# Optimization experiments

Measured on AMD Instinct MI355X. Metric: run time of the kernel, lower is better.

Reference implementation:

```python
import jax, jax.numpy as jnp
import numpy as np

H = 2048
D = 128            # align_dim
TEMP_TAU = 1.0
BIAS_MAX = 0.5
LN_EPS = 1e-5


def _ln(x, g, b):
    m = jnp.mean(x, axis=-1, keepdims=True)
    v = jnp.mean((x - m) ** 2, axis=-1, keepdims=True)
    return (x - m) / jnp.sqrt(v + LN_EPS) * g + b


def _mlp(x, g, b, W1, b1, W2, b2):
    # LayerNorm -> Linear -> GELU(exact) -> Linear
    h = jax.nn.gelu(_ln(x, g, b) @ W1.T + b1, approximate=False)
    return h @ W2.T + b2


def _l2n(x):
    n = jnp.linalg.norm(x, axis=-1, keepdims=True)
    return x / jnp.maximum(n, 1e-12)


def setup_inputs() -> dict:
    key = jax.random.key(0)
    ks = jax.random.split(key, 20)
    B, L = 4096, 4096
    d2 = 2 * D
    s_h = 1.0 / np.sqrt(H)
    s_d2 = 1.0 / np.sqrt(d2)
    inp = {
        "q": jax.random.normal(ks[0], (B, H), jnp.float32),
        "R_non": jax.random.normal(ks[1], (L, H), jnp.float32),
        # mlp_q
        "ln_q_g": jnp.ones((H,), jnp.float32),
        "ln_q_b": jnp.zeros((H,), jnp.float32),
        "W1q": jax.random.uniform(ks[2], (d2, H), jnp.float32, -s_h, s_h),
        "b1q": jnp.zeros((d2,), jnp.float32),
        "W2q": jax.random.uniform(ks[3], (D, d2), jnp.float32, -s_d2, s_d2),
        "b2q": jnp.zeros((D,), jnp.float32),
        # mlp_r
        "ln_r_g": jnp.ones((H,), jnp.float32),
        "ln_r_b": jnp.zeros((H,), jnp.float32),
        "W1r": jax.random.uniform(ks[4], (d2, H), jnp.float32, -s_h, s_h),
        "b1r": jnp.zeros((d2,), jnp.float32),
        "W2r": jax.random.uniform(ks[5], (D, d2), jnp.float32, -s_d2, s_d2),
        "b2r": jnp.zeros((D,), jnp.float32),
        # mlp_dec (input 2D=256 -> 128 -> 1)
        "ln_d_g": jnp.ones((d2,), jnp.float32),
        "ln_d_b": jnp.zeros((d2,), jnp.float32),
        "W1d": jax.random.uniform(ks[6], (128, d2), jnp.float32, -s_d2, s_d2),
        "b1d": jnp.zeros((128,), jnp.float32),
        "W2d": jax.random.uniform(ks[7], (1, 128), jnp.float32, -1 / np.sqrt(128), 1 / np.sqrt(128)),
        "b2d": jnp.zeros((1,), jnp.float32),
        # scalar heads
        "beta": jax.random.uniform(ks[8], (2,), jnp.float32, -0.1, 0.1),
        "W_len": jax.random.uniform(ks[9], (1, 2), jnp.float32, -0.1, 0.1),
        "b_len": jnp.zeros((1,), jnp.float32),
    }
    return inp


def reference(q, R_non, ln_q_g, ln_q_b, W1q, b1q, W2q, b2q,
              ln_r_g, ln_r_b, W1r, b1r, W2r, b2r,
              ln_d_g, ln_d_b, W1d, b1d, W2d, b2d,
              beta, W_len, b_len):
    L = R_non.shape[0]
    z_q = _l2n(_mlp(q, ln_q_g, ln_q_b, W1q, b1q, W2q, b2q))          # [B, D]
    Z_r = _l2n(_mlp(R_non, ln_r_g, ln_r_b, W1r, b1r, W2r, b2r))      # [L, D]
    scores = (z_q @ Z_r.T) / jnp.sqrt(jnp.float32(D))                 # [B, L]
    attn = jax.nn.softmax(scores, axis=-1)                            # [B, L]
    r_bar = _l2n(attn @ Z_r)                                          # [B, D]
    inter = jnp.concatenate([z_q, r_bar], axis=-1)                    # [B, 2D]
    raw_logit = _mlp(inter, ln_d_g, ln_d_b, W1d, b1d, W2d, b2d)[..., 0]  # [B]
    cos_q_r = jnp.sum(z_q * r_bar, axis=-1)                           # [B]
    entropy = -jnp.sum(attn * jnp.log(attn + 1e-8), axis=-1)          # [B]
    u_n = entropy / jnp.log(jnp.float32(L))                           # [B]
    sf = jnp.stack([cos_q_r, u_n], axis=-1)                           # [B, 2]
    delta_len_norm = (sf @ W_len.T + b_len)[..., 0]                   # [B]
    len_feat = jnp.tanh(delta_len_norm / TEMP_TAU)
    delta_theta = jnp.clip(beta[0] * u_n + beta[1] * len_feat, -BIAS_MAX, BIAS_MAX)
    return raw_logit, delta_theta
```

## Files before the change

kernel.cpp:

```cpp
#include <hip/hip_runtime.h>
#include <math.h>


#define HD   2048
#define D2   256
#define DD   128
#define NQ   4096
#define NT   8192
#define NSPLIT 16
#define KPS  (NQ / NSPLIT)
#define NIT  (KPS / 64)

typedef __attribute__((ext_vector_type(8))) short s16x8;
typedef __attribute__((ext_vector_type(4))) float f32x4;

static __device__ __forceinline__ float gelu_exact(float x){
    return 0.5f * x * (1.0f + erff(x * 0.7071067811865475f));
}
static __device__ __forceinline__ unsigned short f2bf(float f){
    unsigned int u = __float_as_uint(f);
    return (unsigned short)((u + 0x7FFFu + ((u >> 16) & 1u)) >> 16);
}
static __device__ __forceinline__ unsigned int pack2bf(float a, float b){
    return (unsigned int)f2bf(a) | ((unsigned int)f2bf(b) << 16);
}

static __device__ __forceinline__ void gload_lds16(const void* g, void* l){
    __builtin_amdgcn_global_load_lds(
        (const __attribute__((address_space(1))) unsigned int*)g,
        (__attribute__((address_space(3))) unsigned int*)l, 16, 0, 0);
}

__global__ __launch_bounds__(256)
void kLN_cast(const float* __restrict__ q, const float* __restrict__ R,
              const float* __restrict__ gq, const float* __restrict__ bq,
              const float* __restrict__ gr, const float* __restrict__ br,
              const float* __restrict__ W1q, const float* __restrict__ W1r,
              unsigned short* __restrict__ Xbf, unsigned short* __restrict__ Wbf){
    const int r = blockIdx.x;
    const int tid = threadIdx.x;
    if (r >= NT){
        const int rw = r - NT;
        const float* src = (rw >= 256) ? (W1r + (size_t)(rw - 256) * HD)
                                       : (W1q + (size_t)rw * HD);
        float4 a = *(const float4*)&src[tid * 8];
        float4 c = *(const float4*)&src[tid * 8 + 4];
        uint4 p = {pack2bf(a.x, a.y), pack2bf(a.z, a.w),
                   pack2bf(c.x, c.y), pack2bf(c.z, c.w)};
        *(uint4*)&Wbf[(size_t)rw * HD + tid * 8] = p;
        return;
    }
    const float* src = (r < NQ) ? (q + (size_t)r * HD) : (R + (size_t)(r - NQ) * HD);
    const float* g  = (r < NQ) ? gq : gr;
    const float* bb = (r < NQ) ? bq : br;
    float4 x0 = *(const float4*)&src[tid * 8];
    float4 x1 = *(const float4*)&src[tid * 8 + 4];
    float v[8] = {x0.x, x0.y, x0.z, x0.w, x1.x, x1.y, x1.z, x1.w};
    float s = 0.f, sq = 0.f;
#pragma unroll
    for (int i = 0; i < 8; ++i){ s += v[i]; sq += v[i] * v[i]; }
#pragma unroll
    for (int off = 32; off > 0; off >>= 1){
        s  += __shfl_xor(s, off);
        sq += __shfl_xor(sq, off);
    }
    __shared__ float wS[4], wQ[4];
    const int wave = tid >> 6, lane = tid & 63;
    if (lane == 0){ wS[wave] = s; wQ[wave] = sq; }
    __syncthreads();
    float sum = wS[0] + wS[1] + wS[2] + wS[3];
    float sqs = wQ[0] + wQ[1] + wQ[2] + wQ[3];
    float mean = sum * (1.0f / HD);
    float var  = sqs * (1.0f / HD) - mean * mean;
    float rstd = rsqrtf(fmaxf(var, 0.0f) + 1e-5f);
    float4 g0 = *(const float4*)&g[tid * 8];
    float4 g1 = *(const float4*)&g[tid * 8 + 4];
    float4 b0 = *(const float4*)&bb[tid * 8];
    float4 b1 = *(const float4*)&bb[tid * 8 + 4];
    float gg[8] = {g0.x, g0.y, g0.z, g0.w, g1.x, g1.y, g1.z, g1.w};
    float bv[8] = {b0.x, b0.y, b0.z, b0.w, b1.x, b1.y, b1.z, b1.w};
    float h[8];
#pragma unroll
    for (int i = 0; i < 8; ++i) h[i] = (v[i] - mean) * rstd * gg[i] + bv[i];
    uint4 p = {pack2bf(h[0], h[1]), pack2bf(h[2], h[3]),
               pack2bf(h[4], h[5]), pack2bf(h[6], h[7])};
    *(uint4*)&Xbf[(size_t)r * HD + tid * 8] = p;
}

__global__ __launch_bounds__(256)
void k2_mfma(const unsigned short* __restrict__ Xbf,
             const unsigned short* __restrict__ Wbf,
             float* __restrict__ HP){
    const int tid  = threadIdx.x;
    const int wave = tid >> 6, lane = tid & 63;
    const int quad = lane >> 4, col = lane & 15;
    const int mblk = blockIdx.x;
    const int nblk = blockIdx.y;
    const int ks   = blockIdx.z;
    const int inp  = mblk >> 6;
    const int mbase = mblk * 64;
    const int nbase = nblk * 128;
    const int wm = wave & 1, wn = wave >> 1;

    __shared__ __align__(16) char smem[49152];

    const unsigned short* gA[2];
    const unsigned short* gB[4];
#pragma unroll
    for (int i = 0; i < 2; ++i){
        int s = i * 256 + wave * 64 + lane;
        int row = s >> 3, c = (s & 7) ^ (row & 7);
        gA[i] = Xbf + (size_t)(mbase + row) * HD + ks * 1024 + c * 8;
    }
#pragma unroll
    for (int j = 0; j < 4; ++j){
        int s = j * 256 + wave * 64 + lane;
        int row = s >> 3, c = (s & 7) ^ (row & 7);
        gB[j] = Wbf + (size_t)(inp * 256 + nbase + row) * HD + ks * 1024 + c * 8;
    }

#define K2_STAGE(d, k0)                                                        \
    {                                                                          \
        _Pragma("unroll")                                                      \
        for (int i = 0; i < 2; ++i)                                            \
            gload_lds16(gA[i] + (k0),                                          \
                        smem + (d) * 24576 + (i * 256 + wave * 64 + lane) * 16);\
        _Pragma("unroll")                                                      \
        for (int j = 0; j < 4; ++j)                                            \
            gload_lds16(gB[j] + (k0),                                          \
                        smem + (d) * 24576 + 8192 + (j * 256 + wave * 64 + lane) * 16);\
    }

    int aoff[2][2], boff[4][2];
#pragma unroll
    for (int mi = 0; mi < 2; ++mi){
        int ra = wm * 32 + mi * 16 + col;
#pragma unroll
        for (int kst = 0; kst < 2; ++kst){
            int cc = kst * 4 + quad;
            aoff[mi][kst] = ra * 128 + ((cc ^ (ra & 7)) << 4);
        }
    }
#pragma unroll
    for (int ni = 0; ni < 4; ++ni){
        int rb = wn * 64 + ni * 16 + col;
#pragma unroll
        for (int kst = 0; kst < 2; ++kst){
            int cc = kst * 4 + quad;
            boff[ni][kst] = rb * 128 + ((cc ^ (rb & 7)) << 4);
        }
    }

    f32x4 acc[2][4];
#pragma unroll
    for (int mi = 0; mi < 2; ++mi)
#pragma unroll
        for (int ni = 0; ni < 4; ++ni) acc[mi][ni] = (f32x4){0.f, 0.f, 0.f, 0.f};

    int cur = 0;
    K2_STAGE(0, 0);
    __syncthreads();
    for (int t = 0; t < 16; ++t){
        if (t < 15) K2_STAGE(cur ^ 1, (t + 1) * 64);
        const char* Ab = smem + cur * 24576;
        const char* Bb = Ab + 8192;
        s16x8 a[2][2], b[4][2];
#pragma unroll
        for (int mi = 0; mi < 2; ++mi)
#pragma unroll
            for (int kst = 0; kst < 2; ++kst)
                a[mi][kst] = *(const s16x8*)(Ab + aoff[mi][kst]);
#pragma unroll
        for (int ni = 0; ni < 4; ++ni)
#pragma unroll
            for (int kst = 0; kst < 2; ++kst)
                b[ni][kst] = *(const s16x8*)(Bb + boff[ni][kst]);
#pragma unroll
        for (int kst = 0; kst < 2; ++kst)
#pragma unroll
            for (int mi = 0; mi < 2; ++mi)
#pragma unroll
                for (int ni = 0; ni < 4; ++ni)
                    acc[mi][ni] = __builtin_amdgcn_mfma_f32_16x16x32_bf16(
                        a[mi][kst], b[ni][kst], acc[mi][ni], 0, 0, 0);
        __syncthreads();
        cur ^= 1;
    }
#undef K2_STAGE

    float* dst = HP + (size_t)ks * NT * D2;
#pragma unroll
    for (int mi = 0; mi < 2; ++mi){
#pragma unroll
        for (int ni = 0; ni < 4; ++ni){
#pragma unroll
            for (int reg = 0; reg < 4; ++reg){
                int m = mbase + wm * 32 + mi * 16 + quad * 4 + reg;
                int n = nbase + wn * 64 + ni * 16 + col;
                dst[(size_t)m * D2 + n] = acc[mi][ni][reg];
            }
        }
    }
}

__global__ __launch_bounds__(256)
void k3_gemm2(const float* __restrict__ HP,
              const float* __restrict__ b1q, const float* __restrict__ b1r,
              const float* __restrict__ W2q, const float* __restrict__ b2q,
              const float* __restrict__ W2r, const float* __restrict__ b2r,
              float* __restrict__ Z, unsigned short* __restrict__ Zbf){
    const int gstart = blockIdx.x * 16;
    const int inp = (gstart >= NQ) ? 1 : 0;
    const float* b1 = inp ? b1r : b1q;
    const float* W2 = inp ? W2r : W2q;
    const float* b2 = inp ? b2r : b2q;

    __shared__ __align__(16) float Hs[16][68];
    __shared__ __align__(16) float Wk[64][132];
    __shared__ float red[16][17];
    __shared__ float normS[16];

    const int tid = threadIdx.x;
    const int ty = tid >> 4;
    const int tx = tid & 15;

    float acc[8];
#pragma unroll
    for (int jj = 0; jj < 8; ++jj) acc[jj] = 0.f;

    for (int kc = 0; kc < 4; ++kc){
#pragma unroll
        for (int i = 0; i < 4; ++i){
            int e = tid + i * 256;
            int rr = e >> 6, kk = e & 63;
            size_t idx = (size_t)(gstart + rr) * D2 + kc * 64 + kk;
            float hv = HP[idx] + HP[(size_t)NT * D2 + idx] + b1[kc * 64 + kk];
            Hs[rr][kk] = gelu_exact(hv);
        }
#pragma unroll
        for (int i = 0; i < 32; ++i){
            int e = tid + i * 256;
            int nn = e >> 6, kk = e & 63;
            Wk[kk][nn] = W2[(size_t)nn * D2 + kc * 64 + kk];
        }
        __syncthreads();
#pragma unroll
        for (int k4 = 0; k4 < 16; ++k4){
            float a0[4];
            float4 t0 = *(const float4*)&Hs[ty][k4 * 4];
            a0[0] = t0.x; a0[1] = t0.y; a0[2] = t0.z; a0[3] = t0.w;
#pragma unroll
            for (int kq = 0; kq < 4; ++kq){
                float4 w0 = *(const float4*)&Wk[k4 * 4 + kq][tx * 8];
                float4 w1 = *(const float4*)&Wk[k4 * 4 + kq][tx * 8 + 4];
                float wv[8] = {w0.x, w0.y, w0.z, w0.w, w1.x, w1.y, w1.z, w1.w};
#pragma unroll
                for (int jj = 0; jj < 8; ++jj)
                    acc[jj] += a0[kq] * wv[jj];
            }
        }
        __syncthreads();
    }
    float v0[8];
    float sq0 = 0.f;
#pragma unroll
    for (int jj = 0; jj < 8; ++jj){
        int c = tx * 8 + jj;
        v0[jj] = acc[jj] + b2[c];
        sq0 += v0[jj] * v0[jj];
    }
    red[ty][tx] = sq0;
    __syncthreads();
    if (tid < 16){
        float s = 0.f;
#pragma unroll
        for (int t = 0; t < 16; ++t) s += red[tid][t];
        normS[tid] = 1.0f / fmaxf(sqrtf(s), 1e-12f);
    }
    __syncthreads();
    float s0 = normS[ty];
    int row0 = gstart + ty;
    size_t o0 = (size_t)row0 * DD + tx * 8;
    float z0[8];
#pragma unroll
    for (int jj = 0; jj < 8; ++jj) z0[jj] = v0[jj] * s0;
    float4 a = {z0[0], z0[1], z0[2], z0[3]}, b = {z0[4], z0[5], z0[6], z0[7]};
    *(float4*)&Z[o0]     = a;  *(float4*)&Z[o0 + 4] = b;
    uint4 p0 = {pack2bf(z0[0], z0[1]), pack2bf(z0[2], z0[3]),
                pack2bf(z0[4], z0[5]), pack2bf(z0[6], z0[7])};
    *(uint4*)&Zbf[o0] = p0;
}

__global__ __launch_bounds__(256)
void kT_transpose(const unsigned short* __restrict__ Zbf,
                  unsigned short* __restrict__ ZbfT){
    __shared__ unsigned short Ts[64][129];
    const int r0 = blockIdx.x * 64;
    const int tid = threadIdx.x;
#pragma unroll
    for (int i = 0; i < 32; ++i){
        int e = tid + i * 256;
        int rr = e >> 7, dd = e & 127;
        Ts[rr][dd] = Zbf[(size_t)(NQ + r0 + rr) * DD + dd];
    }
    __syncthreads();
#pragma unroll
    for (int i = 0; i < 32; ++i){
        int e = tid + i * 256;
        int dd = e >> 6, rr = e & 63;
        ZbfT[(size_t)dd * NQ + r0 + rr] = Ts[rr][dd];
    }
}

__global__ __launch_bounds__(256)
void kA_attn(const unsigned short* __restrict__ Zbf,
             const unsigned short* __restrict__ ZbfT,
             float* __restrict__ OP, float* __restrict__ LW){
    const int tid  = threadIdx.x;
    const int wave = tid >> 6, lane = tid & 63;
    const int quad = lane >> 4, col = lane & 15;
    const int m0   = blockIdx.x * 128 + wave * 32;
    const int split = blockIdx.y;
    const float scl = 0.08838834764831845f;

    __shared__ __align__(16) char sK[16384];
    __shared__ __align__(16) char sV[16384];
    __shared__ __align__(16) unsigned short Pt[4][2][16][72];

    s16x8 aq[2][4];
#pragma unroll
    for (int m = 0; m < 2; ++m)
#pragma unroll
        for (int kb = 0; kb < 4; ++kb)
            aq[m][kb] = *(const s16x8*)&Zbf[(size_t)(m0 + m * 16 + col) * DD + kb * 32 + quad * 8];

    const unsigned short* gK[4];
    const unsigned short* gV[4];
    int dK[4], dV[4];
#pragma unroll
    for (int i = 0; i < 4; ++i){
        int s = i * 256 + tid;
        int row = s >> 4, c = (s & 15) ^ (row & 15);
        gK[i] = Zbf + (size_t)(NQ + row) * DD + c * 8;
        dK[i] = s * 16;
        int s2 = i * 256 + tid;
        int rv = s2 >> 3, cv = (s2 & 7) ^ (rv & 7);
        gV[i] = ZbfT + (size_t)rv * NQ + cv * 8;
        dV[i] = s2 * 16;
    }

    int kOff[4][4];
#pragma unroll
    for (int nt = 0; nt < 4; ++nt){
        int rb = nt * 16 + col;
#pragma unroll
        for (int kb = 0; kb < 4; ++kb)
            kOff[nt][kb] = rb * 256 + (((kb * 4 + quad) ^ (rb & 15)) << 4);
    }
    int vOff[8][2];
#pragma unroll
    for (int dt = 0; dt < 8; ++dt){
        int rv = dt * 16 + col;
#pragma unroll
        for (int kb2 = 0; kb2 < 2; ++kb2)
            vOff[dt][kb2] = rv * 128 + (((kb2 * 4 + quad) ^ (rv & 7)) << 4);
    }

    f32x4 o[2][8];
#pragma unroll
    for (int m = 0; m < 2; ++m)
#pragma unroll
        for (int dt = 0; dt < 8; ++dt) o[m][dt] = (f32x4){0.f, 0.f, 0.f, 0.f};
    float lp[2][4] = {{0.f,0.f,0.f,0.f},{0.f,0.f,0.f,0.f}};
    float wp[2][4] = {{0.f,0.f,0.f,0.f},{0.f,0.f,0.f,0.f}};

    for (int it = 0; it < NIT; ++it){
        const int r0 = split * KPS + it * 64;
#pragma unroll
        for (int i = 0; i < 4; ++i)
            gload_lds16(gK[i] + (size_t)r0 * DD, sK + dK[i]);
#pragma unroll
        for (int i = 0; i < 4; ++i)
            gload_lds16(gV[i] + r0, sV + dV[i]);
        __syncthreads();

#pragma unroll
        for (int nt = 0; nt < 4; ++nt){
            s16x8 b[4];
#pragma unroll
            for (int kb = 0; kb < 4; ++kb)
                b[kb] = *(const s16x8*)(sK + kOff[nt][kb]);
#pragma unroll
            for (int m = 0; m < 2; ++m){
                f32x4 s = (f32x4){0.f, 0.f, 0.f, 0.f};
#pragma unroll
                for (int kb = 0; kb < 4; ++kb)
                    s = __builtin_amdgcn_mfma_f32_16x16x32_bf16(aq[m][kb], b[kb], s, 0, 0, 0);
#pragma unroll
                for (int reg = 0; reg < 4; ++reg){
                    float sv = s[reg] * scl;
                    float e  = __expf(sv);
                    lp[m][reg] += e;
                    wp[m][reg] += e * sv;
                    Pt[wave][m][quad * 4 + reg][nt * 16 + col] = f2bf(e);
                }
            }
        }

        s16x8 ap[2][2];
#pragma unroll
        for (int m = 0; m < 2; ++m)
#pragma unroll
            for (int kb2 = 0; kb2 < 2; ++kb2)
                ap[m][kb2] = *(const s16x8*)&Pt[wave][m][col][kb2 * 32 + quad * 8];
#pragma unroll
        for (int dt = 0; dt < 8; ++dt){
#pragma unroll
            for (int kb2 = 0; kb2 < 2; ++kb2){
                s16x8 b = *(const s16x8*)(sV + vOff[dt][kb2]);
                o[0][dt] = __builtin_amdgcn_mfma_f32_16x16x32_bf16(ap[0][kb2], b, o[0][dt], 0, 0, 0);
                o[1][dt] = __builtin_amdgcn_mfma_f32_16x16x32_bf16(ap[1][kb2], b, o[1][dt], 0, 0, 0);
            }
        }
        __syncthreads();
    }

#pragma unroll
    for (int m = 0; m < 2; ++m)
#pragma unroll
    for (int reg = 0; reg < 4; ++reg){
        float l = lp[m][reg], w = wp[m][reg];
        l += __shfl_xor(l, 8);  w += __shfl_xor(w, 8);
        l += __shfl_xor(l, 4);  w += __shfl_xor(w, 4);
        l += __shfl_xor(l, 2);  w += __shfl_xor(w, 2);
        l += __shfl_xor(l, 1);  w += __shfl_xor(w, 1);
        if (col == 0){
            int row = m0 + m * 16 + quad * 4 + reg;
            LW[((size_t)split * NQ + row) * 2]     = l;
            LW[((size_t)split * NQ + row) * 2 + 1] = w;
        }
    }
#pragma unroll
    for (int m = 0; m < 2; ++m)
#pragma unroll
    for (int dt = 0; dt < 8; ++dt){
#pragma unroll
        for (int reg = 0; reg < 4; ++reg){
            int row = m0 + m * 16 + quad * 4 + reg;
            OP[((size_t)split * NQ + row) * DD + dt * 16 + col] = o[m][dt][reg];
        }
    }
}

__global__ __launch_bounds__(128)
void kC_combine(const float* __restrict__ OP, const float* __restrict__ LW,
                const float* __restrict__ Z,
                float* __restrict__ RB, float* __restrict__ COS,
                float* __restrict__ ILW){
    const int r = blockIdx.x;
    const int c = threadIdx.x;
    const int lane = c & 63, wv = c >> 6;
    float v = 0.f;
#pragma unroll
    for (int s = 0; s < NSPLIT; ++s) v += OP[((size_t)s * NQ + r) * DD + c];

    __shared__ float sred[2][2];
    float t = v * v;
#pragma unroll
    for (int off = 32; off > 0; off >>= 1) t += __shfl_xor(t, off);
    if (lane == 0) sred[0][wv] = t;
    __syncthreads();
    float scale = 1.0f / fmaxf(sqrtf(sred[0][0] + sred[0][1]), 1e-12f);
    float rb = v * scale;
    RB[(size_t)r * DD + c] = rb;
    float zq = Z[(size_t)r * DD + c];
    float cz = zq * rb;
#pragma unroll
    for (int off = 32; off > 0; off >>= 1) cz += __shfl_xor(cz, off);
    if (lane == 0) sred[1][wv] = cz;

    float l_p = 0.f, w_p = 0.f;
    if (c < NSPLIT){
        l_p = LW[((size_t)c * NQ + r) * 2];
        w_p = LW[((size_t)c * NQ + r) * 2 + 1];
    }
#pragma unroll
    for (int off = 8; off > 0; off >>= 1){
        l_p += __shfl_xor(l_p, off);
        w_p += __shfl_xor(w_p, off);
    }
    __syncthreads();
    if (c == 0){
        COS[r] = sred[1][0] + sred[1][1];
        float ent = logf(l_p) - w_p / l_p;
        ILW[2 * r]     = 1.0f / l_p;
        ILW[2 * r + 1] = ent * (1.0f / 8.317766166719343f);
    }
}

__global__ __launch_bounds__(256)
void k8_decoder(const float* __restrict__ Z, const float* __restrict__ RB,
                const float* __restrict__ ILW, const float* __restrict__ COS,
                const float* __restrict__ gd, const float* __restrict__ bd,
                const float* __restrict__ W1d, const float* __restrict__ b1d,
                const float* __restrict__ W2d, const float* __restrict__ b2d,
                const float* __restrict__ beta, const float* __restrict__ W_len,
                const float* __restrict__ b_len,
                float* __restrict__ out){
    const int r0 = blockIdx.x * 4;
    const int tid = threadIdx.x;
    const int wave = tid >> 6, lane = tid & 63;

    __shared__ __align__(16) float Xs[4][256];
    __shared__ __align__(16) float Wd[128][33];
    __shared__ float pr[4][2];

    {
        const int row = r0 + wave;
        const int c0 = lane * 4;
        float4 v;
        if (c0 < DD) v = *(const float4*)&Z[(size_t)row * DD + c0];
        else         v = *(const float4*)&RB[(size_t)row * DD + (c0 - DD)];
        float s  = v.x + v.y + v.z + v.w;
        float sq = v.x * v.x + v.y * v.y + v.z * v.z + v.w * v.w;
#pragma unroll
        for (int off = 32; off > 0; off >>= 1){
            s  += __shfl_xor(s, off);
            sq += __shfl_xor(sq, off);
        }
        float mean = s * (1.0f / D2);
        float var  = sq * (1.0f / D2) - mean * mean;
        float rstd = rsqrtf(fmaxf(var, 0.0f) + 1e-5f);
        float4 g = *(const float4*)&gd[c0];
        float4 b = *(const float4*)&bd[c0];
        float4 xn;
        xn.x = (v.x - mean) * rstd * g.x + b.x;
        xn.y = (v.y - mean) * rstd * g.y + b.y;
        xn.z = (v.z - mean) * rstd * g.z + b.z;
        xn.w = (v.w - mean) * rstd * g.w + b.w;
        *(float4*)&Xs[wave][c0] = xn;
    }
    __syncthreads();

    const int j  = tid & 127;
    const int rp = tid >> 7;
    const float* xa = &Xs[rp * 2][0];
    const float* xb = &Xs[rp * 2 + 1][0];
    float h0 = 0.f, h1 = 0.f;
    for (int cch = 0; cch < 8; ++cch){
#pragma unroll
        for (int i = 0; i < 16; ++i){
            int e = tid + i * 256;
            int j2 = e >> 5, kk = e & 31;
            Wd[j2][kk] = W1d[(size_t)j2 * D2 + cch * 32 + kk];
        }
        __syncthreads();
#pragma unroll
        for (int k4 = 0; k4 < 8; ++k4){
            float4 w  = *(const float4*)&Wd[j][k4 * 4];
            float4 a4 = *(const float4*)&xa[cch * 32 + k4 * 4];
            float4 b4 = *(const float4*)&xb[cch * 32 + k4 * 4];
            h0 += w.x * a4.x + w.y * a4.y + w.z * a4.z + w.w * a4.w;
            h1 += w.x * b4.x + w.y * b4.y + w.z * b4.z + w.w * b4.w;
        }
        __syncthreads();
    }
    float bj = b1d[j];
    h0 = gelu_exact(h0 + bj);
    h1 = gelu_exact(h1 + bj);
    float w2 = W2d[j];
    float p0 = h0 * w2, p1 = h1 * w2;
#pragma unroll
    for (int off = 32; off > 0; off >>= 1){
        p0 += __shfl_xor(p0, off);
        p1 += __shfl_xor(p1, off);
    }
    if (lane == 0){ pr[wave][0] = p0; pr[wave][1] = p1; }
    __syncthreads();

    if (tid < 4){
        const int row   = tid;
        const int rpair = row >> 1, rlo = row & 1;
        float lg = b2d[0] + pr[rpair * 2][rlo] + pr[rpair * 2 + 1][rlo];
        const int gr = r0 + row;
        float u  = ILW[2 * gr + 1];
        float cv = COS[gr];
        float dln = cv * W_len[0] + u * W_len[1] + b_len[0];
        float dt = beta[0] * u + beta[1] * tanhf(dln);
        dt = fminf(0.5f, fmaxf(-0.5f, dt));
        out[gr]      = lg;
        out[NQ + gr] = dt;
    }
}

extern "C" void kernel_launch(void* const* d_in, const int* in_sizes, int n_in,
                              void* d_out, int out_size, void* d_ws, size_t ws_size,
                              hipStream_t stream){
    const float* q      = (const float*)d_in[0];
    const float* R      = (const float*)d_in[1];
    const float* ln_q_g = (const float*)d_in[2];
    const float* ln_q_b = (const float*)d_in[3];
    const float* W1q    = (const float*)d_in[4];
    const float* b1q    = (const float*)d_in[5];
    const float* W2q    = (const float*)d_in[6];
    const float* b2q    = (const float*)d_in[7];
    const float* ln_r_g = (const float*)d_in[8];
    const float* ln_r_b = (const float*)d_in[9];
    const float* W1r    = (const float*)d_in[10];
    const float* b1r    = (const float*)d_in[11];
    const float* W2r    = (const float*)d_in[12];
    const float* b2r    = (const float*)d_in[13];
    const float* ln_d_g = (const float*)d_in[14];
    const float* ln_d_b = (const float*)d_in[15];
    const float* W1d    = (const float*)d_in[16];
    const float* b1d    = (const float*)d_in[17];
    const float* W2d    = (const float*)d_in[18];
    const float* b2d    = (const float*)d_in[19];
    const float* beta   = (const float*)d_in[20];
    const float* W_len  = (const float*)d_in[21];
    const float* b_len  = (const float*)d_in[22];

    float* WS = (float*)d_ws;
    unsigned short* Xbf  = (unsigned short*)(WS);
    float* OP    = WS;
    float* HP    = WS + 8388608;
    float* LW    = WS + 8388608;
    unsigned short* Wbf  = (unsigned short*)(WS + 12582912);
    float* Z     = WS + 13107200;
    unsigned short* Zbf  = (unsigned short*)(WS + 14155776);
    unsigned short* ZbfT = (unsigned short*)(WS + 14680064);
    float* RB    = WS + 14942208;
    float* COSV  = WS + 15466496;
    float* ILW   = WS + 15470592;
    float* out   = (float*)d_out;

    hipLaunchKernelGGL(kLN_cast, dim3(NT + 512), dim3(256), 0, stream,
                       q, R, ln_q_g, ln_q_b, ln_r_g, ln_r_b, W1q, W1r, Xbf, Wbf);
    hipLaunchKernelGGL(k2_mfma, dim3(128, 2, 2), dim3(256), 0, stream, Xbf, Wbf, HP);
    hipLaunchKernelGGL(k3_gemm2, dim3(512), dim3(256), 0, stream,
                       HP, b1q, b1r, W2q, b2q, W2r, b2r, Z, Zbf);
    hipLaunchKernelGGL(kT_transpose, dim3(64), dim3(256), 0, stream, Zbf, ZbfT);
    hipLaunchKernelGGL(kA_attn, dim3(32, NSPLIT), dim3(256), 0, stream, Zbf, ZbfT, OP, LW);
    hipLaunchKernelGGL(kC_combine, dim3(NQ), dim3(128), 0, stream, OP, LW, Z, RB, COSV, ILW);
    hipLaunchKernelGGL(k8_decoder, dim3(1024), dim3(256), 0, stream,
                       Z, RB, ILW, COSV, ln_d_g, ln_d_b, W1d, b1d, W2d, b2d,
                       beta, W_len, b_len, out);
}
```

Baseline: 247.7 us.

## Fuse split-combine into decoder kernel and store partials row-major by split

Removes the separate combine kernel and folds the reduction of the attention split partials (output sum, L2 normalisation, cosine, entropy) into the decoder kernel, keeping r_bar in shared memory instead of writing it to global. The partial output and log-sum buffers are relaid so each row's splits are contiguous, which makes the per-row gather in the decoder a contiguous read. This saves one launch and an RB/COS/ILW round trip through global memory. The attention kernel's stores become more scattered in exchange.

```diff
diff --git a/kernel.cpp b/kernel.cpp
--- a/kernel.cpp
+++ b/kernel.cpp
@@ -436,8 +436,8 @@
         l += __shfl_xor(l, 1);  w += __shfl_xor(w, 1);
         if (col == 0){
             int row = m0 + m * 16 + quad * 4 + reg;
-            LW[((size_t)split * NQ + row) * 2]     = l;
-            LW[((size_t)split * NQ + row) * 2 + 1] = w;
+            LW[((size_t)row * NSPLIT + split) * 2]     = l;
+            LW[((size_t)row * NSPLIT + split) * 2 + 1] = w;
         }
     }
 #pragma unroll
@@ -447,60 +447,14 @@
 #pragma unroll
         for (int reg = 0; reg < 4; ++reg){
             int row = m0 + m * 16 + quad * 4 + reg;
-            OP[((size_t)split * NQ + row) * DD + dt * 16 + col] = o[m][dt][reg];
-        }
-    }
-}
-
-__global__ __launch_bounds__(128)
-void kC_combine(const float* __restrict__ OP, const float* __restrict__ LW,
-                const float* __restrict__ Z,
-                float* __restrict__ RB, float* __restrict__ COS,
-                float* __restrict__ ILW){
-    const int r = blockIdx.x;
-    const int c = threadIdx.x;
-    const int lane = c & 63, wv = c >> 6;
-    float v = 0.f;
-#pragma unroll
-    for (int s = 0; s < NSPLIT; ++s) v += OP[((size_t)s * NQ + r) * DD + c];
-
-    __shared__ float sred[2][2];
-    float t = v * v;
-#pragma unroll
-    for (int off = 32; off > 0; off >>= 1) t += __shfl_xor(t, off);
-    if (lane == 0) sred[0][wv] = t;
-    __syncthreads();
-    float scale = 1.0f / fmaxf(sqrtf(sred[0][0] + sred[0][1]), 1e-12f);
-    float rb = v * scale;
-    RB[(size_t)r * DD + c] = rb;
-    float zq = Z[(size_t)r * DD + c];
-    float cz = zq * rb;
-#pragma unroll
-    for (int off = 32; off > 0; off >>= 1) cz += __shfl_xor(cz, off);
-    if (lane == 0) sred[1][wv] = cz;
-
-    float l_p = 0.f, w_p = 0.f;
-    if (c < NSPLIT){
-        l_p = LW[((size_t)c * NQ + r) * 2];
-        w_p = LW[((size_t)c * NQ + r) * 2 + 1];
-    }
-#pragma unroll
-    for (int off = 8; off > 0; off >>= 1){
-        l_p += __shfl_xor(l_p, off);
-        w_p += __shfl_xor(w_p, off);
-    }
-    __syncthreads();
-    if (c == 0){
-        COS[r] = sred[1][0] + sred[1][1];
-        float ent = logf(l_p) - w_p / l_p;
-        ILW[2 * r]     = 1.0f / l_p;
-        ILW[2 * r + 1] = ent * (1.0f / 8.317766166719343f);
+            OP[((size_t)row * NSPLIT + split) * DD + dt * 16 + col] = o[m][dt][reg];
+        }
     }
 }
 
 __global__ __launch_bounds__(256)
-void k8_decoder(const float* __restrict__ Z, const float* __restrict__ RB,
-                const float* __restrict__ ILW, const float* __restrict__ COS,
+void k8_decoder(const float* __restrict__ Z, const float* __restrict__ OP,
+                const float* __restrict__ LW,
                 const float* __restrict__ gd, const float* __restrict__ bd,
                 const float* __restrict__ W1d, const float* __restrict__ b1d,
                 const float* __restrict__ W2d, const float* __restrict__ b2d,
@@ -510,17 +464,56 @@
     const int r0 = blockIdx.x * 4;
     const int tid = threadIdx.x;
     const int wave = tid >> 6, lane = tid & 63;
+    const int row = r0 + wave;
 
     __shared__ __align__(16) float Xs[4][256];
     __shared__ __align__(16) float Wd[128][33];
+    __shared__ float RBs[4][128];
     __shared__ float pr[4][2];
+    __shared__ float cosS[4], uS[4];
 
     {
-        const int row = r0 + wave;
+        const int c0 = lane * 2;
+        float v0 = 0.f, v1 = 0.f;
+#pragma unroll
+        for (int s = 0; s < NSPLIT; ++s){
+            float2 t = *(const float2*)&OP[((size_t)row * NSPLIT + s) * DD + c0];
+            v0 += t.x; v1 += t.y;
+        }
+        float ss = v0 * v0 + v1 * v1;
+#pragma unroll
+        for (int off = 32; off > 0; off >>= 1) ss += __shfl_xor(ss, off);
+        float scale = 1.0f / fmaxf(sqrtf(ss), 1e-12f);
+        float rb0 = v0 * scale, rb1 = v1 * scale;
+        RBs[wave][c0]     = rb0;
+        RBs[wave][c0 + 1] = rb1;
+        float2 zq = *(const float2*)&Z[(size_t)row * DD + c0];
+        float cz = zq.x * rb0 + zq.y * rb1;
+#pragma unroll
+        for (int off = 32; off > 0; off >>= 1) cz += __shfl_xor(cz, off);
+        float l_p = 0.f, w_p = 0.f;
+        if (lane < NSPLIT){
+            float2 lw = *(const float2*)&LW[((size_t)row * NSPLIT + lane) * 2];
+            l_p = lw.x; w_p = lw.y;
+        }
+#pragma unroll
+        for (int off = 8; off > 0; off >>= 1){
+            l_p += __shfl_xor(l_p, off);
+            w_p += __shfl_xor(w_p, off);
+        }
+        if (lane == 0){
+            cosS[wave] = cz;
+            float ent = logf(l_p) - w_p / l_p;
+            uS[wave] = ent * (1.0f / 8.317766166719343f);
+        }
+    }
+    __syncthreads();
+
+    {
         const int c0 = lane * 4;
         float4 v;
         if (c0 < DD) v = *(const float4*)&Z[(size_t)row * DD + c0];
-        else         v = *(const float4*)&RB[(size_t)row * DD + (c0 - DD)];
+        else         v = *(const float4*)&RBs[wave][c0 - DD];
         float s  = v.x + v.y + v.z + v.w;
         float sq = v.x * v.x + v.y * v.y + v.z * v.z + v.w * v.w;
 #pragma unroll
@@ -579,12 +572,12 @@
     __syncthreads();
 
     if (tid < 4){
-        const int row   = tid;
-        const int rpair = row >> 1, rlo = row & 1;
+        const int rw    = tid;
+        const int rpair = rw >> 1, rlo = rw & 1;
         float lg = b2d[0] + pr[rpair * 2][rlo] + pr[rpair * 2 + 1][rlo];
-        const int gr = r0 + row;
-        float u  = ILW[2 * gr + 1];
-        float cv = COS[gr];
+        const int gr = r0 + rw;
+        float u  = uS[rw];
+        float cv = cosS[rw];
         float dln = cv * W_len[0] + u * W_len[1] + b_len[0];
         float dt = beta[0] * u + beta[1] * tanhf(dln);
         dt = fminf(0.5f, fmaxf(-0.5f, dt));
@@ -629,9 +622,6 @@
     float* Z     = WS + 13107200;
     unsigned short* Zbf  = (unsigned short*)(WS + 14155776);
     unsigned short* ZbfT = (unsigned short*)(WS + 14680064);
-    float* RB    = WS + 14942208;
-    float* COSV  = WS + 15466496;
-    float* ILW   = WS + 15470592;
     float* out   = (float*)d_out;
 
     hipLaunchKernelGGL(kLN_cast, dim3(NT + 512), dim3(256), 0, stream,
@@ -641,8 +631,7 @@
                        HP, b1q, b1r, W2q, b2q, W2r, b2r, Z, Zbf);
     hipLaunchKernelGGL(kT_transpose, dim3(64), dim3(256), 0, stream, Zbf, ZbfT);
     hipLaunchKernelGGL(kA_attn, dim3(32, NSPLIT), dim3(256), 0, stream, Zbf, ZbfT, OP, LW);
-    hipLaunchKernelGGL(kC_combine, dim3(NQ), dim3(128), 0, stream, OP, LW, Z, RB, COSV, ILW);
     hipLaunchKernelGGL(k8_decoder, dim3(1024), dim3(256), 0, stream,
-                       Z, RB, ILW, COSV, ln_d_g, ln_d_b, W1d, b1d, W2d, b2d,
+                       Z, OP, LW, ln_d_g, ln_d_b, W1d, b1d, W2d, b2d,
                        beta, W_len, b_len, out);
 }
```

Result: faster. 242.5 us (-2.1%).
